# Performance work log

Hardware: AMD Instinct MI355X
Metric: run time of the kernel (lower is better)

The kernel has to match this reference:

```python
import jax, jax.numpy as jnp
import numpy as np


def log_g(x):
    # log of g(x) = x + 0.5 for x>=0, sigmoid(x) for x<0
    return jnp.where(x >= 0, jnp.log(jnp.maximum(x, 0) + 0.5), -jax.nn.softplus(-x))


def setup_inputs() -> dict:
    key = jax.random.key(0)
    k_x, k_w, k_o, k_b = jax.random.split(key, 4)
    B, S, D, H, O = 4, 8192, 1024, 1024, 1024
    x = jax.random.normal(k_x, (B, S, D), dtype=jnp.float32)
    # torch Linear weights: [out_features, in_features]
    w_in = jax.random.normal(k_w, (3 * H, D), dtype=jnp.float32) / np.sqrt(D)
    w_out = jax.random.normal(k_o, (O, H), dtype=jnp.float32) / np.sqrt(H)
    b_out = jax.random.normal(k_b, (O,), dtype=jnp.float32) * 0.01
    return {"x": x, "w_in": w_in, "w_out": w_out, "b_out": b_out}


def reference(x, w_in, w_out, b_out):
    B, S, D = x.shape
    H = w_in.shape[0] // 3
    z = jnp.einsum('bsd,hd->bsh', x, w_in)          # [B, S, 3H]
    f, i, h = jnp.split(z, 3, axis=-1)
    diff = jax.nn.softplus(-f) - jax.nn.softplus(-i)
    log_f = -jax.nn.softplus(diff)                  # [B, S, H]
    log_i = -jax.nn.softplus(-diff)
    log_h0 = jnp.full((B, 1, H), jnp.log(0.5), dtype=x.dtype)  # log_g(0)
    log_tilde_h = log_g(h)
    # NOTE: faithful to source -- cumsum is applied over a singleton dim
    # (identity), so a_star is just [0, log_f] along seq (no prefix sum).
    a_star = jnp.concatenate([jnp.zeros((B, 1, H), dtype=x.dtype), log_f], axis=1)  # [B, S+1, H]
    log_val = jnp.concatenate([log_h0, log_i + log_tilde_h], axis=1)                # [B, S+1, H]
    log_h = a_star + jax.lax.cumlogsumexp(log_val - a_star, axis=1)
    h_t = jnp.exp(log_h)                            # [B, S+1, H]
    out = h_t[:, -1, :] @ w_out.T + b_out           # [B, O]
    return out
```

## Files before the change

kernel.cpp:

```cpp
#include <hip/hip_runtime.h>
#include <math.h>

constexpr int B_ = 4, S_ = 8192, D_ = 1024, H_ = 1024, O_ = 1024;

typedef float f32x4  __attribute__((ext_vector_type(4)));
typedef float f32x16 __attribute__((ext_vector_type(16)));
typedef int   i32x4  __attribute__((ext_vector_type(4)));
typedef int   i32x8  __attribute__((ext_vector_type(8)));

__device__ __forceinline__ float softplusf(float x) {
    if (x > 20.f) return x;
    if (x < -20.f) return expf(x);
    return log1pf(expf(x));
}

__global__ __launch_bounds__(256) void cvt_fp8_2(
    const float* __restrict__ srcA, unsigned char* __restrict__ dstA, int nA8,
    const float* __restrict__ srcB, unsigned char* __restrict__ dstB, int nB8) {
    int i = blockIdx.x * blockDim.x + threadIdx.x;
    const float* src; unsigned char* dst; float sc;
    if (i < nA8) { src = srcA; dst = dstA; sc = 1.f; }
    else { i -= nA8; if (i >= nB8) return; src = srcB; dst = dstB; sc = 16.f; }
    const float4* s = (const float4*)src + (size_t)i * 2;
    float4 a = s[0], b = s[1];
    int lo = __builtin_amdgcn_cvt_pk_fp8_f32(a.x * sc, a.y * sc, 0, false);
    lo     = __builtin_amdgcn_cvt_pk_fp8_f32(a.z * sc, a.w * sc, lo, true);
    int hi = __builtin_amdgcn_cvt_pk_fp8_f32(b.x * sc, b.y * sc, 0, false);
    hi     = __builtin_amdgcn_cvt_pk_fp8_f32(b.z * sc, b.w * sc, hi, true);
    ((int2*)dst)[i] = make_int2(lo, hi);
}

__global__ __launch_bounds__(256) void f_exact(
    const float* __restrict__ x, const float* __restrict__ w_in,
    float* __restrict__ F_ws)
{
    const int lane = threadIdx.x & 63;
    const int pair = blockIdx.x * 4 + (threadIdx.x >> 6);
    const int b = pair >> 10, h = pair & (H_ - 1);
    const float* xr = x + ((size_t)b * S_ + (S_ - 1)) * D_;
    const float* wf = w_in + (size_t)h * D_;
    const float* wi = wf + (size_t)H_ * D_;
    float sf = 0.f, si = 0.f;
    for (int k = lane; k < D_; k += 64) {
        float xv = xr[k];
        sf = fmaf(xv, wf[k], sf);
        si = fmaf(xv, wi[k], si);
    }
    #pragma unroll
    for (int off = 32; off > 0; off >>= 1) {
        sf += __shfl_xor(sf, off, 64);
        si += __shfl_xor(si, off, 64);
    }
    if (lane == 0) {
        float af1 = 1.f + expf(-sf), ai1 = 1.f + expf(-si);
        F_ws[(size_t)b * H_ + h] = ai1 / (af1 + ai1);
    }
}

constexpr int BM = 256, BN = 64, BK = 64;
constexpr int ABYTES = BM * BK;
constexpr int BUF_BYTES = (BM + 3 * BN) * BK;
constexpr int NX = B_ * S_ * D_;

__global__ __launch_bounds__(256, 2) void gemm_fused_fp8(
    const unsigned char* __restrict__ xq, const unsigned char* __restrict__ wq,
    float* __restrict__ acc_ws)
{
    __shared__ __align__(16) unsigned char sbuf[2][BUF_BYTES];
    __shared__ float colsum[BN];

    const int id = blockIdx.x;
    const int c8 = id & 7;
    const int q  = id >> 3;
    const int hb = q & 15;
    const int pl = q >> 4;
    const int panel = c8 * 16 + pl;
    const int sb = panel & 31;
    const int b  = panel >> 5;

    const int h0   = hb * BN;
    const int s0   = sb * BM;
    const int tid  = threadIdx.x;
    const int lane = tid & 63;
    const int wid  = tid >> 6;
    const int wm   = wid >> 1;
    const int wn   = wid & 1;
    const int l31  = lane & 31;
    const int half = lane >> 5;

    if (tid < BN) colsum[tid] = 0.f;

    int goff[7];
    {
        const int rl = lane >> 2;
        const int sp = lane & 3;
        const int qq = sp ^ ((rl >> 1) & 3);
        #pragma unroll
        for (int j = 0; j < 7; ++j) {
            int u = wid * 7 + j;
            if (u < 16) {
                int row = u * 16 + rl;
                goff[j] = (b * S_ + s0 + row) * D_ + qq * 16;
            } else {
                int v = u - 16;
                int row = (v & 3) * 16 + rl;
                goff[j] = NX + (v >> 2) * (H_ * D_) + (h0 + row) * D_ + qq * 16;
            }
        }
    }
    const int wbase = wid * 7 * 1024;

    const int g2 = (l31 >> 1) & 3;
    const int sA = ((half * 2) ^ g2) * 16;
    const int aof0  = (wm * 128 + l31) * 64 + sA;
    const int aof0x = aof0 ^ 16;
    const int bof0  = ABYTES + (wn * 32 + l31) * 64 + sA;
    const int bof0x = bof0 ^ 16;

    f32x16 acc[3][4] = {};

    auto issue_loads = [&](int nxt) {
        #pragma unroll
        for (int j = 0; j < 7; ++j) {
            __builtin_amdgcn_global_load_lds(
                (const __attribute__((address_space(1))) void*)(xq + goff[j]),
                (__attribute__((address_space(3))) void*)(&sbuf[nxt][wbase + j * 1024]),
                16, 0, 0);
            goff[j] += BK;
        }
    };
    auto rd8 = [](const unsigned char* base, int o0, int o1) -> i32x8 {
        i32x4 lo = *(const i32x4*)(base + o0);
        i32x4 hi = *(const i32x4*)(base + o1);
        i32x8 r = {lo.x, lo.y, lo.z, lo.w, hi.x, hi.y, hi.z, hi.w};
        return r;
    };
    auto compute = [&](int cur) {
        const unsigned char* bp = &sbuf[cur][0];
        i32x8 af[4];
        #pragma unroll
        for (int t = 0; t < 4; ++t)
            af[t] = rd8(bp, aof0 + t * 2048, aof0x + t * 2048);
        #pragma unroll
        for (int g = 0; g < 3; ++g) {
            i32x8 bf = rd8(bp, bof0 + g * 4096, bof0x + g * 4096);
            #pragma unroll
            for (int t = 0; t < 4; ++t)
                acc[g][t] = __builtin_amdgcn_mfma_scale_f32_32x32x64_f8f6f4(
                    af[t], bf, acc[g][t],
                    0, 0,
                    0, 0x7F7F7F7F,
                    0, 0x7B7B7B7B);
        }
    };

    constexpr int NC = D_ / BK;
    issue_loads(0);
    issue_loads(1);
    #pragma unroll
    for (int c = 0; c < NC - 1; ++c) {
        asm volatile("s_waitcnt vmcnt(7)" ::: "memory");
        __builtin_amdgcn_s_barrier();
        __builtin_amdgcn_s_setprio(1);
        compute(c & 1);
        __builtin_amdgcn_s_setprio(0);
        asm volatile("s_waitcnt lgkmcnt(0)" ::: "memory");
        __builtin_amdgcn_sched_barrier(0);
        __builtin_amdgcn_s_barrier();
        if (c + 2 < NC) issue_loads(c & 1);
    }
    asm volatile("s_waitcnt vmcnt(0)" ::: "memory");
    __builtin_amdgcn_s_barrier();
    __builtin_amdgcn_s_setprio(1);
    compute((NC - 1) & 1);
    __builtin_amdgcn_s_setprio(0);

    float vsum = 0.f;
    #pragma unroll
    for (int t = 0; t < 4; ++t) {
        f32x16 fv = acc[0][t], iv = acc[1][t], hv = acc[2][t];
        #pragma unroll
        for (int r = 0; r < 16; ++r) {
            float ef = __expf(-fv[r]);
            float ei = __expf(-iv[r]);
            float h  = hv[r];
            float eh = __expf(h);
            float g  = (h >= 0.f) ? (h + 0.5f)
                                  : (eh * __builtin_amdgcn_rcpf(1.f + eh));
            vsum += (1.f + ef) * __builtin_amdgcn_rcpf(1.f + ei) * g;
        }
    }
    vsum += __shfl_xor(vsum, 32, 64);
    if (half == 0) atomicAdd(&colsum[wn * 32 + l31], vsum);
    __syncthreads();
    if (tid < BN)
        atomicAdd(&acc_ws[(size_t)b * H_ + h0 + tid], colsum[tid]);
}

__global__ __launch_bounds__(256) void out_gemv(
    const float* __restrict__ wout, const float* __restrict__ bout,
    const float* __restrict__ acc_ws, const float* __restrict__ F_ws,
    float* __restrict__ out)
{
    const int lane = threadIdx.x & 63;
    const int o = blockIdx.x * 4 + (threadIdx.x >> 6);
    float s[B_] = {};
    for (int h = lane; h < H_; h += 64) {
        float w = wout[(size_t)o * H_ + h];
        #pragma unroll
        for (int b = 0; b < B_; ++b) {
            float hv = F_ws[b * H_ + h] * (0.5f + acc_ws[b * H_ + h]);
            s[b] = fmaf(w, hv, s[b]);
        }
    }
    #pragma unroll
    for (int b = 0; b < B_; ++b)
        #pragma unroll
        for (int off = 32; off > 0; off >>= 1)
            s[b] += __shfl_down(s[b], off, 64);
    if (lane == 0) {
        float bo = bout[o];
        #pragma unroll
        for (int b = 0; b < B_; ++b)
            out[(size_t)b * O_ + o] = s[b] + bo;
    }
}

constexpr int TS = 64, TH = 64, TK = 16, LDP = 68;

__global__ __launch_bounds__(256) void fused_gemm_reduce(
    const float* __restrict__ x, const float* __restrict__ win,
    float* __restrict__ acc_ws, float* __restrict__ F_ws)
{
    __shared__ __align__(16) float As[TK][LDP];
    __shared__ __align__(16) float Wf[TK][LDP];
    __shared__ __align__(16) float Wi[TK][LDP];
    __shared__ __align__(16) float Wh[TK][LDP];
    __shared__ float colsum[TH];

    const int b  = blockIdx.z;
    const int s0 = blockIdx.x * TS;
    const int h0 = blockIdx.y * TH;
    const int tid = threadIdx.x;
    const int tx = tid & 15;
    const int ty = tid >> 4;

    float accf[4][4] = {};
    float acci[4][4] = {};
    float acch[4][4] = {};

    const int lrow = tid >> 2;
    const int lk4  = (tid & 3) << 2;

    const float* xp  = x   + ((size_t)b * S_ + (s0 + lrow)) * D_ + lk4;
    const float* wfp = win + (size_t)(h0 + lrow) * D_ + lk4;
    const float* wip = wfp + (size_t)H_ * D_;
    const float* whp = wip + (size_t)H_ * D_;

    for (int k0 = 0; k0 < D_; k0 += TK) {
        float4 va = *(const float4*)(xp  + k0);
        float4 vf = *(const float4*)(wfp + k0);
        float4 vi = *(const float4*)(wip + k0);
        float4 vh = *(const float4*)(whp + k0);
        __syncthreads();
        As[lk4+0][lrow]=va.x; As[lk4+1][lrow]=va.y; As[lk4+2][lrow]=va.z; As[lk4+3][lrow]=va.w;
        Wf[lk4+0][lrow]=vf.x; Wf[lk4+1][lrow]=vf.y; Wf[lk4+2][lrow]=vf.z; Wf[lk4+3][lrow]=vf.w;
        Wi[lk4+0][lrow]=vi.x; Wi[lk4+1][lrow]=vi.y; Wi[lk4+2][lrow]=vi.z; Wi[lk4+3][lrow]=vi.w;
        Wh[lk4+0][lrow]=vh.x; Wh[lk4+1][lrow]=vh.y; Wh[lk4+2][lrow]=vh.z; Wh[lk4+3][lrow]=vh.w;
        __syncthreads();
        #pragma unroll
        for (int k = 0; k < TK; ++k) {
            float4 a4 = *(const float4*)&As[k][ty << 2];
            float4 f4 = *(const float4*)&Wf[k][tx << 2];
            float4 i4 = *(const float4*)&Wi[k][tx << 2];
            float4 h4 = *(const float4*)&Wh[k][tx << 2];
            float a[4]  = {a4.x, a4.y, a4.z, a4.w};
            float wf[4] = {f4.x, f4.y, f4.z, f4.w};
            float wi[4] = {i4.x, i4.y, i4.z, i4.w};
            float wh[4] = {h4.x, h4.y, h4.z, h4.w};
            #pragma unroll
            for (int r = 0; r < 4; ++r)
                #pragma unroll
                for (int cc = 0; cc < 4; ++cc) {
                    accf[r][cc] = fmaf(a[r], wf[cc], accf[r][cc]);
                    acci[r][cc] = fmaf(a[r], wi[cc], acci[r][cc]);
                    acch[r][cc] = fmaf(a[r], wh[cc], acch[r][cc]);
                }
        }
    }

    const bool last_s = (s0 + TS == S_);
    float cval[4] = {0.f, 0.f, 0.f, 0.f};
    #pragma unroll
    for (int cc = 0; cc < 4; ++cc)
        #pragma unroll
        for (int r = 0; r < 4; ++r) {
            float f = accf[r][cc], i = acci[r][cc], h = acch[r][cc];
            float d  = softplusf(-f) - softplusf(-i);
            float lg = (h >= 0.f) ? logf(h + 0.5f) : -softplusf(-h);
            cval[cc] += expf(d + lg);
            if (last_s && ty == 15 && r == 3)
                F_ws[(size_t)b * H_ + h0 + (tx << 2) + cc] = expf(-softplusf(d));
        }
    if (tid < TH) colsum[tid] = 0.f;
    __syncthreads();
    #pragma unroll
    for (int cc = 0; cc < 4; ++cc)
        atomicAdd(&colsum[(tx << 2) + cc], cval[cc]);
    __syncthreads();
    if (tid < TH)
        atomicAdd(&acc_ws[(size_t)b * H_ + h0 + tid], colsum[tid]);
}

extern "C" void kernel_launch(void* const* d_in, const int* in_sizes, int n_in,
                              void* d_out, int out_size, void* d_ws, size_t ws_size,
                              hipStream_t stream) {
    const float* x    = (const float*)d_in[0];
    const float* w_in = (const float*)d_in[1];
    const float* wout = (const float*)d_in[2];
    const float* bout = (const float*)d_in[3];
    float* out = (float*)d_out;

    float* acc_ws = (float*)d_ws;
    float* F_ws   = acc_ws + (size_t)B_ * H_;

    hipMemsetAsync(d_ws, 0, 2 * (size_t)B_ * H_ * sizeof(float), stream);

    const size_t nx = (size_t)B_ * S_ * D_;
    const size_t nw = (size_t)3 * H_ * D_;
    const size_t q_off = 32768;
    const size_t need = q_off + nx + nw;

    if (ws_size >= need) {
        unsigned char* xq = (unsigned char*)d_ws + q_off;
        unsigned char* wq = xq + nx;
        int nx8 = (int)(nx / 8), nw8 = (int)(nw / 8);
        cvt_fp8_2<<<(nx8 + nw8 + 255) / 256, 256, 0, stream>>>(
            x, xq, nx8, w_in, wq, nw8);
        f_exact<<<B_ * H_ / 4, 256, 0, stream>>>(x, w_in, F_ws);
        gemm_fused_fp8<<<(H_ / BN) * (S_ / BM) * B_, 256, 0, stream>>>(
            xq, wq, acc_ws);
    } else {
        dim3 grid(S_ / TS, H_ / TH, B_);
        fused_gemm_reduce<<<grid, 256, 0, stream>>>(x, w_in, acc_ws, F_ws);
    }
    out_gemv<<<O_ / 4, 256, 0, stream>>>(wout, bout, acc_ws, F_ws, out);
}
```

Baseline: 330.6 us.

## Deepen FP8 GEMM pipeline to four LDS buffers with 512 threads and fragment prefetch

The fused FP8 GEMM moves from 256 to 512 threads per block, giving each of eight waves a smaller share of the tile (2 M-subtiles instead of 4). Shared memory grows from a static double buffer to a four-stage dynamic buffer with DMA issued three chunks ahead. Register fragments are ping-ponged so the next chunk's LDS reads overlap the current MFMAs. This aims to hide global-load and LDS latency better, at the cost of more LDS per block, which may lower residency, and more complex wait-count bookkeeping.

```diff
diff --git a/kernel.cpp b/kernel.cpp
--- a/kernel.cpp
+++ b/kernel.cpp
@@ -60,14 +60,14 @@
 constexpr int BM = 256, BN = 64, BK = 64;
 constexpr int ABYTES = BM * BK;
 constexpr int BUF_BYTES = (BM + 3 * BN) * BK;
-constexpr int NX = B_ * S_ * D_;
-
-__global__ __launch_bounds__(256, 2) void gemm_fused_fp8(
+constexpr int NBUF = 4;
+constexpr int SMEM_BYTES = NBUF * BUF_BYTES;
+
+__global__ __launch_bounds__(512, 2) void gemm_fused_fp8(
     const unsigned char* __restrict__ xq, const unsigned char* __restrict__ wq,
     float* __restrict__ acc_ws)
 {
-    __shared__ __align__(16) unsigned char sbuf[2][BUF_BYTES];
-    __shared__ float colsum[BN];
+    extern __shared__ unsigned char smem[];
 
     const int id = blockIdx.x;
     const int c8 = id & 7;
@@ -88,45 +88,49 @@
     const int l31  = lane & 31;
     const int half = lane >> 5;
 
-    if (tid < BN) colsum[tid] = 0.f;
-
-    int goff[7];
+    const unsigned char* gp[4];
     {
         const int rl = lane >> 2;
         const int sp = lane & 3;
         const int qq = sp ^ ((rl >> 1) & 3);
         #pragma unroll
-        for (int j = 0; j < 7; ++j) {
-            int u = wid * 7 + j;
+        for (int j = 0; j < 4; ++j) {
+            int u = wid * 4 + j;
             if (u < 16) {
                 int row = u * 16 + rl;
-                goff[j] = (b * S_ + s0 + row) * D_ + qq * 16;
-            } else {
+                gp[j] = xq + (size_t)(b * S_ + s0 + row) * D_ + qq * 16;
+            } else if (u < 28) {
                 int v = u - 16;
                 int row = (v & 3) * 16 + rl;
-                goff[j] = NX + (v >> 2) * (H_ * D_) + (h0 + row) * D_ + qq * 16;
+                gp[j] = wq + (size_t)(v >> 2) * (H_ * D_)
+                           + (size_t)(h0 + row) * D_ + qq * 16;
+            } else {
+                gp[j] = xq;
             }
         }
     }
-    const int wbase = wid * 7 * 1024;
+    const int wbase = wid * 4 * 1024;
 
     const int g2 = (l31 >> 1) & 3;
     const int sA = ((half * 2) ^ g2) * 16;
-    const int aof0  = (wm * 128 + l31) * 64 + sA;
+    const int aof0  = (wm * 64 + l31) * 64 + sA;
     const int aof0x = aof0 ^ 16;
     const int bof0  = ABYTES + (wn * 32 + l31) * 64 + sA;
     const int bof0x = bof0 ^ 16;
 
-    f32x16 acc[3][4] = {};
-
-    auto issue_loads = [&](int nxt) {
-        #pragma unroll
-        for (int j = 0; j < 7; ++j) {
-            __builtin_amdgcn_global_load_lds(
-                (const __attribute__((address_space(1))) void*)(xq + goff[j]),
-                (__attribute__((address_space(3))) void*)(&sbuf[nxt][wbase + j * 1024]),
-                16, 0, 0);
-            goff[j] += BK;
+    f32x16 acc[3][2] = {};
+
+    auto issue_dma = [&](int c) {
+        if (wid < 7) {
+            unsigned char* lb = smem + (c & 3) * BUF_BYTES + wbase;
+            #pragma unroll
+            for (int j = 0; j < 4; ++j) {
+                __builtin_amdgcn_global_load_lds(
+                    (const __attribute__((address_space(1))) void*)gp[j],
+                    (__attribute__((address_space(3))) void*)(lb + j * 1024),
+                    16, 0, 0);
+                gp[j] += BK;
+            }
         }
     };
     auto rd8 = [](const unsigned char* base, int o0, int o1) -> i32x8 {
@@ -135,49 +139,69 @@
         i32x8 r = {lo.x, lo.y, lo.z, lo.w, hi.x, hi.y, hi.z, hi.w};
         return r;
     };
-    auto compute = [&](int cur) {
-        const unsigned char* bp = &sbuf[cur][0];
-        i32x8 af[4];
-        #pragma unroll
-        for (int t = 0; t < 4; ++t)
-            af[t] = rd8(bp, aof0 + t * 2048, aof0x + t * 2048);
-        #pragma unroll
-        for (int g = 0; g < 3; ++g) {
-            i32x8 bf = rd8(bp, bof0 + g * 4096, bof0x + g * 4096);
+    auto ld_frags = [&](int c, i32x8* af, i32x8* bf) {
+        const unsigned char* bp = smem + (c & 3) * BUF_BYTES;
+        af[0] = rd8(bp, aof0,        aof0x);
+        af[1] = rd8(bp, aof0 + 2048, aof0x + 2048);
+        bf[0] = rd8(bp, bof0,        bof0x);
+        bf[1] = rd8(bp, bof0 + 4096, bof0x + 4096);
+        bf[2] = rd8(bp, bof0 + 8192, bof0x + 8192);
+    };
+    auto do_mfma = [&](const i32x8* af, const i32x8* bf) {
+        __builtin_amdgcn_s_setprio(1);
+        #pragma unroll
+        for (int g = 0; g < 3; ++g)
             #pragma unroll
-            for (int t = 0; t < 4; ++t)
+            for (int t = 0; t < 2; ++t)
                 acc[g][t] = __builtin_amdgcn_mfma_scale_f32_32x32x64_f8f6f4(
-                    af[t], bf, acc[g][t],
+                    af[t], bf[g], acc[g][t],
                     0, 0,
                     0, 0x7F7F7F7F,
                     0, 0x7B7B7B7B);
-        }
+        __builtin_amdgcn_s_setprio(0);
     };
 
+    i32x8 afE[2], bfE[3], afO[2], bfO[3];
+
+    issue_dma(0); issue_dma(1); issue_dma(2);
+    asm volatile("s_waitcnt vmcnt(8)" ::: "memory");
+    __builtin_amdgcn_sched_barrier(0);
+    __builtin_amdgcn_s_barrier();
+    ld_frags(0, afE, bfE);
+    asm volatile("s_waitcnt vmcnt(4) lgkmcnt(0)" ::: "memory");
+    __builtin_amdgcn_sched_barrier(0);
+    __builtin_amdgcn_s_barrier();
+
     constexpr int NC = D_ / BK;
-    issue_loads(0);
-    issue_loads(1);
-    #pragma unroll
-    for (int c = 0; c < NC - 1; ++c) {
-        asm volatile("s_waitcnt vmcnt(7)" ::: "memory");
-        __builtin_amdgcn_s_barrier();
-        __builtin_amdgcn_s_setprio(1);
-        compute(c & 1);
-        __builtin_amdgcn_s_setprio(0);
-        asm volatile("s_waitcnt lgkmcnt(0)" ::: "memory");
-        __builtin_amdgcn_sched_barrier(0);
-        __builtin_amdgcn_s_barrier();
-        if (c + 2 < NC) issue_loads(c & 1);
-    }
-    asm volatile("s_waitcnt vmcnt(0)" ::: "memory");
-    __builtin_amdgcn_s_barrier();
-    __builtin_amdgcn_s_setprio(1);
-    compute((NC - 1) & 1);
-    __builtin_amdgcn_s_setprio(0);
+    #pragma unroll
+    for (int c = 0; c < NC; ++c) {
+        i32x8* afC = (c & 1) ? afO : afE;
+        i32x8* bfC = (c & 1) ? bfO : bfE;
+        i32x8* afN = (c & 1) ? afE : afO;
+        i32x8* bfN = (c & 1) ? bfE : bfO;
+        if (c + 1 < NC) ld_frags(c + 1, afN, bfN);
+        if (c + 3 < NC) issue_dma(c + 3);
+        do_mfma(afC, bfC);
+        if (c + 1 < NC) {
+            if (c + 3 < NC)
+                asm volatile("s_waitcnt vmcnt(4) lgkmcnt(0)" ::: "memory");
+            else if (c == NC - 3)
+                asm volatile("s_waitcnt vmcnt(0) lgkmcnt(0)" ::: "memory");
+            else
+                asm volatile("s_waitcnt lgkmcnt(0)" ::: "memory");
+            __builtin_amdgcn_sched_barrier(0);
+            __builtin_amdgcn_s_barrier();
+        }
+    }
+
+    __syncthreads();
+    float* colsum = (float*)smem;
+    if (tid < BN) colsum[tid] = 0.f;
+    __syncthreads();
 
     float vsum = 0.f;
     #pragma unroll
-    for (int t = 0; t < 4; ++t) {
+    for (int t = 0; t < 2; ++t) {
         f32x16 fv = acc[0][t], iv = acc[1][t], hv = acc[2][t];
         #pragma unroll
         for (int r = 0; r < 16; ++r) {
@@ -335,10 +359,18 @@
         unsigned char* xq = (unsigned char*)d_ws + q_off;
         unsigned char* wq = xq + nx;
         int nx8 = (int)(nx / 8), nw8 = (int)(nw / 8);
+
+        static int attr_done = 0;
+        if (!attr_done) {
+            (void)hipFuncSetAttribute((const void*)gemm_fused_fp8,
+                hipFuncAttributeMaxDynamicSharedMemorySize, SMEM_BYTES);
+            attr_done = 1;
+        }
+
         cvt_fp8_2<<<(nx8 + nw8 + 255) / 256, 256, 0, stream>>>(
             x, xq, nx8, w_in, wq, nw8);
         f_exact<<<B_ * H_ / 4, 256, 0, stream>>>(x, w_in, F_ws);
-        gemm_fused_fp8<<<(H_ / BN) * (S_ / BM) * B_, 256, 0, stream>>>(
+        gemm_fused_fp8<<<(H_ / BN) * ((B_ * S_) / BM), 512, SMEM_BYTES, stream>>>(
             xq, wq, acc_ws);
     } else {
         dim3 grid(S_ / TS, H_ / TH, B_);
```

Result: no change. 331.4 us (+0.3%).
